# Kernel optimization log

Hardware: AMD Instinct MI355X
Metric: run time of the kernel (lower is better)

## Reference

```python
import jax, jax.numpy as jnp
import numpy as np

N = 100000          # num nodes
E = 1600000         # num edges
IN_F = 256
OUT_F = 256
D_LABEL = 32
ALPHA = 0.2         # LeakyReLU negative slope
EPS = 1e-9


def setup_inputs() -> dict:
    key = jax.random.key(0)
    k1, k2, k3, k4 = jax.random.split(key, 4)
    h = jax.random.normal(k1, (N, IN_F), dtype=jnp.float32)
    label = jax.random.normal(k2, (N, D_LABEL), dtype=jnp.float32)
    # xavier_uniform with gain=1.414 on [IN_F, OUT_F]
    limit = 1.414 * np.sqrt(6.0 / (IN_F + OUT_F))
    W = jax.random.uniform(k3, (IN_F, OUT_F), dtype=jnp.float32,
                           minval=-limit, maxval=limit)
    adj_indices = jax.random.randint(k4, (2, E), 0, N, dtype=jnp.int64)
    return {"h": h, "label": label, "W": W, "adj_indices": adj_indices}


def reference(h, label, W, adj_indices):
    src = adj_indices[0]  # [E]
    dst = adj_indices[1]  # [E]
    Wh = h @ W  # [N, OUT_F]
    # edge attention logits: leakyrelu(<label[src], label[dst]>)
    e = jnp.sum(label[src] * label[dst], axis=1)            # [E]
    e = jnp.where(e >= 0, e, ALPHA * e)                     # LeakyReLU
    # segment softmax over rows (src)
    exp_e = jnp.exp(e)                                      # [E]
    row_sum = jax.ops.segment_sum(exp_e, src, num_segments=N)  # [N]
    row_sum = jnp.maximum(row_sum, EPS)
    att = exp_e / row_sum[src]                              # [E]
    # dropout is identity at inference (training=False)
    # sparse-dense matmul: h_prime[i] = sum_{(i,j) in edges} att * Wh[j]
    msgs = att[:, None] * Wh[dst]                           # [E, OUT_F]
    h_prime = jax.ops.segment_sum(msgs, src, num_segments=N)  # [N, OUT_F]
    return h_prime  # concat=False -> no ELU
```

## Files before the change

kernel.cpp:

```cpp
#include <hip/hip_runtime.h>
#include <hip/hip_bf16.h>

#define NNODES 100000
#define NEDGES 1600000
#define ALPHA  0.2f
#define EPSV   1e-9f

typedef __bf16 bf16x8 __attribute__((ext_vector_type(8)));
typedef float  f32x4  __attribute__((ext_vector_type(4)));
typedef unsigned short u16x8 __attribute__((ext_vector_type(8)));

static __device__ inline unsigned short f2bf(float f) {
    unsigned int u = __float_as_uint(f);
    unsigned int r = u + 0x7fff + ((u >> 16) & 1);
    return (unsigned short)(r >> 16);
}
static __device__ inline float bf2f(unsigned short v) {
    return __uint_as_float((unsigned int)v << 16);
}

__global__ void k_zero(int* __restrict__ p, int n) {
    int i = blockIdx.x * blockDim.x + threadIdx.x;
    if (i < n) p[i] = 0;
}

__global__ void k_prepw(const float* __restrict__ W, unsigned short* __restrict__ Wt) {
    const int i = blockIdx.x * 256 + threadIdx.x;
    const int n = i >> 8, k = i & 255;
    Wt[i] = f2bf(W[k * 256 + n]);
}

#define BM 128
#define BK 32
#define LSTRIDE 40
__global__ __launch_bounds__(256, 2) void k_gemm(const float* __restrict__ h,
                                                 const unsigned short* __restrict__ Wt,
                                                 unsigned short* __restrict__ Wh) {
    __shared__ __align__(16) unsigned short As[BM * LSTRIDE];
    __shared__ __align__(16) unsigned short Bs[256 * LSTRIDE];
    const int tid  = threadIdx.x;
    const int m0   = blockIdx.x * BM;
    const int wave = tid >> 6;
    const int lane = tid & 63;
    const int wm = (wave & 1) * 64;
    const int wn = (wave >> 1) * 128;
    const int fm = lane & 15;
    const int fq = lane >> 4;
    const int fk = fq * 8;

    f32x4 acc[4][8];
    const f32x4 z = {0.f, 0.f, 0.f, 0.f};
#pragma unroll
    for (int i = 0; i < 4; ++i)
#pragma unroll
        for (int j = 0; j < 8; ++j) acc[i][j] = z;

    const int arow = tid >> 1;
    const int acol = (tid & 1) * 16;
    const bool arow_ok = (m0 + arow) < NNODES;
    const float* hrow = h + (size_t)(m0 + arow) * 256 + acol;

    for (int kc = 0; kc < 256; kc += BK) {
        float4 a0, a1, a2, a3;
        if (arow_ok) {
            a0 = *(const float4*)(hrow + kc + 0);
            a1 = *(const float4*)(hrow + kc + 4);
            a2 = *(const float4*)(hrow + kc + 8);
            a3 = *(const float4*)(hrow + kc + 12);
        } else {
            a0 = a1 = a2 = a3 = make_float4(0.f, 0.f, 0.f, 0.f);
        }
        u16x8 bv[4];
#pragma unroll
        for (int q = 0; q < 4; ++q) {
            const int c = tid + 256 * q;
            const int n = c >> 2, koff = (c & 3) * 8;
            bv[q] = *(const u16x8*)(Wt + n * 256 + kc + koff);
        }
        __syncthreads();
        u16x8 p0, p1;
        p0[0]=f2bf(a0.x); p0[1]=f2bf(a0.y); p0[2]=f2bf(a0.z); p0[3]=f2bf(a0.w);
        p0[4]=f2bf(a1.x); p0[5]=f2bf(a1.y); p0[6]=f2bf(a1.z); p0[7]=f2bf(a1.w);
        p1[0]=f2bf(a2.x); p1[1]=f2bf(a2.y); p1[2]=f2bf(a2.z); p1[3]=f2bf(a2.w);
        p1[4]=f2bf(a3.x); p1[5]=f2bf(a3.y); p1[6]=f2bf(a3.z); p1[7]=f2bf(a3.w);
        *(u16x8*)&As[arow * LSTRIDE + acol]     = p0;
        *(u16x8*)&As[arow * LSTRIDE + acol + 8] = p1;
#pragma unroll
        for (int q = 0; q < 4; ++q) {
            const int c = tid + 256 * q;
            const int n = c >> 2, koff = (c & 3) * 8;
            *(u16x8*)&Bs[n * LSTRIDE + koff] = bv[q];
        }
        __syncthreads();
        bf16x8 af[4], bfr[8];
#pragma unroll
        for (int i = 0; i < 4; ++i)
            af[i] = __builtin_bit_cast(bf16x8,
                *(const u16x8*)&As[(wm + 16 * i + fm) * LSTRIDE + fk]);
#pragma unroll
        for (int j = 0; j < 8; ++j)
            bfr[j] = __builtin_bit_cast(bf16x8,
                *(const u16x8*)&Bs[(wn + 16 * j + fm) * LSTRIDE + fk]);
#pragma unroll
        for (int i = 0; i < 4; ++i)
#pragma unroll
            for (int j = 0; j < 8; ++j)
                acc[i][j] = __builtin_amdgcn_mfma_f32_16x16x32_bf16(af[i], bfr[j], acc[i][j], 0, 0, 0);
    }
#pragma unroll
    for (int i = 0; i < 4; ++i) {
#pragma unroll
        for (int r = 0; r < 4; ++r) {
            const int grow = m0 + wm + 16 * i + fq * 4 + r;
            if (grow < NNODES) {
                unsigned short* orow = Wh + (size_t)grow * 256 + wn + fm;
#pragma unroll
                for (int j = 0; j < 8; ++j)
                    orow[16 * j] = f2bf(acc[i][j][r]);
            }
        }
    }
}

__global__ void k_attn(const float* __restrict__ label,
                       const int* __restrict__ src,
                       const int* __restrict__ dst,
                       float* __restrict__ exp_e,
                       int* __restrict__ pos_in_row,
                       int* __restrict__ counts) {
    const int e = blockIdx.x * blockDim.x + threadIdx.x;
    if (e >= NEDGES) return;
    const int s = src[e], d = dst[e];
    const float4* ls = (const float4*)&label[s * 32];
    const float4* ld = (const float4*)&label[d * 32];
    float dot = 0.f;
#pragma unroll
    for (int i = 0; i < 8; ++i) {
        const float4 a = ls[i], b = ld[i];
        dot += a.x * b.x + a.y * b.y + a.z * b.z + a.w * b.w;
    }
    const float lr = dot >= 0.f ? dot : ALPHA * dot;
    exp_e[e] = expf(lr);
    pos_in_row[e] = atomicAdd(&counts[s], 1);
}

__global__ __launch_bounds__(256) void k_scan1(const int* __restrict__ counts,
                                               int* __restrict__ row_start,
                                               int* __restrict__ blockSums) {
    __shared__ int ssum[256];
    const int tid = threadIdx.x;
    const int base = blockIdx.x * 1024 + tid * 4;
    int v[4];
#pragma unroll
    for (int c = 0; c < 4; ++c) v[c] = (base + c < NNODES) ? counts[base + c] : 0;
    const int s = v[0] + v[1] + v[2] + v[3];
    ssum[tid] = s;
    __syncthreads();
    for (int off = 1; off < 256; off <<= 1) {
        const int t = (tid >= off) ? ssum[tid - off] : 0;
        __syncthreads();
        ssum[tid] += t;
        __syncthreads();
    }
    if (tid == 255) blockSums[blockIdx.x] = ssum[255];
    int p = ssum[tid] - s;
#pragma unroll
    for (int c = 0; c < 4; ++c) {
        if (base + c < NNODES) row_start[base + c] = p;
        p += v[c];
    }
}

__global__ __launch_bounds__(256) void k_scan2(int* __restrict__ blockSums, int nb) {
    __shared__ int ssum[256];
    const int tid = threadIdx.x;
    const int s = (tid < nb) ? blockSums[tid] : 0;
    ssum[tid] = s;
    __syncthreads();
    for (int off = 1; off < 256; off <<= 1) {
        const int t = (tid >= off) ? ssum[tid - off] : 0;
        __syncthreads();
        ssum[tid] += t;
        __syncthreads();
    }
    if (tid < nb) blockSums[tid] = ssum[tid] - s;
}

__global__ void k_scan3(int* __restrict__ row_start, const int* __restrict__ blockSums) {
    const int i = blockIdx.x * blockDim.x + threadIdx.x;
    if (i < NNODES) row_start[i] += blockSums[i >> 10];
}

__global__ void k_scatter(const int* __restrict__ src,
                          const int* __restrict__ dst,
                          const float* __restrict__ exp_e,
                          const int* __restrict__ pos_in_row,
                          const int* __restrict__ row_start,
                          int* __restrict__ sorted_dst,
                          float* __restrict__ sorted_w) {
    const int e = blockIdx.x * blockDim.x + threadIdx.x;
    if (e >= NEDGES) return;
    const int pos = row_start[src[e]] + pos_in_row[e];
    sorted_dst[pos] = dst[e];
    sorted_w[pos] = exp_e[e];
}

__global__ __launch_bounds__(256) void k_aggregate(const unsigned short* __restrict__ Wh,
                                                   const int* __restrict__ row_start,
                                                   const int* __restrict__ sorted_dst,
                                                   const float* __restrict__ sorted_w,
                                                   float* __restrict__ out) {
    const int node = blockIdx.x * 4 + (threadIdx.x >> 6);
    if (node >= NNODES) return;
    const int lane = threadIdx.x & 63;
    const int rs = row_start[node];
    const int re = (node == NNODES - 1) ? NEDGES : row_start[node + 1];
    float4 acc = make_float4(0.f, 0.f, 0.f, 0.f);
    float wsum = 0.f;
    for (int i = rs; i < re; ++i) {
        const int d = sorted_dst[i];
        const float w = sorted_w[i];
        wsum += w;
        const ushort4 v = *(const ushort4*)&Wh[(size_t)d * 256 + lane * 4];
        acc.x = fmaf(w, bf2f(v.x), acc.x);
        acc.y = fmaf(w, bf2f(v.y), acc.y);
        acc.z = fmaf(w, bf2f(v.z), acc.z);
        acc.w = fmaf(w, bf2f(v.w), acc.w);
    }
    const float inv = 1.f / fmaxf(wsum, EPSV);
    acc.x *= inv; acc.y *= inv; acc.z *= inv; acc.w *= inv;
    *(float4*)&out[(size_t)node * 256 + lane * 4] = acc;
}

extern "C" void kernel_launch(void* const* d_in, const int* in_sizes, int n_in,
                              void* d_out, int out_size, void* d_ws, size_t ws_size,
                              hipStream_t stream) {
    const float* h     = (const float*)d_in[0];
    const float* label = (const float*)d_in[1];
    const float* W     = (const float*)d_in[2];
    const int*   adj   = (const int*)d_in[3];
    const int* src = adj;
    const int* dst = adj + NEDGES;
    float* out = (float*)d_out;

    char* ws = (char*)d_ws;
    unsigned short* Wh  = (unsigned short*)(ws + 0);
    unsigned short* Wt  = (unsigned short*)(ws + 51200000);
    float* exp_e        = (float*)(ws + 51400000);
    int*   pos_in_row   = (int*)  (ws + 57800000);
    float* sorted_w     = (float*)(ws + 64200000);
    int*   sorted_dst   = (int*)  (ws + 70600000);
    int*   counts       = (int*)  (ws + 77000000);
    int*   row_start    = (int*)  (ws + 77400000);
    int*   blockSums    = (int*)  (ws + 77800000);

    k_zero<<<(NNODES + 255) / 256, 256, 0, stream>>>(counts, NNODES);
    k_prepw<<<256, 256, 0, stream>>>(W, Wt);
    k_gemm<<<(NNODES + BM - 1) / BM, 256, 0, stream>>>(h, Wt, Wh);
    k_attn<<<(NEDGES + 255) / 256, 256, 0, stream>>>(label, src, dst, exp_e, pos_in_row, counts);

    const int nb = (NNODES + 1023) / 1024;
    k_scan1<<<nb, 256, 0, stream>>>(counts, row_start, blockSums);
    k_scan2<<<1, 256, 0, stream>>>(blockSums, nb);
    k_scan3<<<(NNODES + 255) / 256, 256, 0, stream>>>(row_start, blockSums);

    k_scatter<<<(NEDGES + 255) / 256, 256, 0, stream>>>(src, dst, exp_e, pos_in_row,
                                                        row_start, sorted_dst, sorted_w);
    k_aggregate<<<(NNODES + 3) / 4, 256, 0, stream>>>(Wh, row_start, sorted_dst, sorted_w, out);
}
```

Before: 517.1 us.

## Split attention dot across lanes, pack sorted edges, widen aggregate loads

The attention kernel now uses four lanes per edge, each reading 8 label floats, and combines the partial dot products with shuffles so each lane issues fewer, better-coalesced loads. The sorted destination index and weight are packed into a single uint2 array, so each edge needs one 8-byte load. The aggregation kernel maps 32 lanes per node with 16-byte bf16 loads and unrolls the edge loop by 4 to keep more gathers in flight. The trade-off is four times as many threads in the attention launch and higher register use in aggregation.

```diff
diff --git a/kernel.cpp b/kernel.cpp
--- a/kernel.cpp
+++ b/kernel.cpp
@@ -122,26 +122,30 @@
     }
 }
 
-__global__ void k_attn(const float* __restrict__ label,
+__global__ __launch_bounds__(256) void k_attn(const float* __restrict__ label,
                        const int* __restrict__ src,
                        const int* __restrict__ dst,
                        float* __restrict__ exp_e,
                        int* __restrict__ pos_in_row,
                        int* __restrict__ counts) {
-    const int e = blockIdx.x * blockDim.x + threadIdx.x;
+    const int t = blockIdx.x * 256 + threadIdx.x;
+    const int e = t >> 2;
+    const int l4 = t & 3;
     if (e >= NEDGES) return;
     const int s = src[e], d = dst[e];
-    const float4* ls = (const float4*)&label[s * 32];
-    const float4* ld = (const float4*)&label[d * 32];
-    float dot = 0.f;
-#pragma unroll
-    for (int i = 0; i < 8; ++i) {
-        const float4 a = ls[i], b = ld[i];
-        dot += a.x * b.x + a.y * b.y + a.z * b.z + a.w * b.w;
-    }
-    const float lr = dot >= 0.f ? dot : ALPHA * dot;
-    exp_e[e] = expf(lr);
-    pos_in_row[e] = atomicAdd(&counts[s], 1);
+    const float4* ls = (const float4*)&label[s * 32 + l4 * 8];
+    const float4* ld = (const float4*)&label[d * 32 + l4 * 8];
+    const float4 a0 = ls[0], a1 = ls[1];
+    const float4 b0 = ld[0], b1 = ld[1];
+    float dot = a0.x * b0.x + a0.y * b0.y + a0.z * b0.z + a0.w * b0.w
+              + a1.x * b1.x + a1.y * b1.y + a1.z * b1.z + a1.w * b1.w;
+    dot += __shfl_xor(dot, 1);
+    dot += __shfl_xor(dot, 2);
+    if (l4 == 0) {
+        const float lr = dot >= 0.f ? dot : ALPHA * dot;
+        exp_e[e] = expf(lr);
+        pos_in_row[e] = atomicAdd(&counts[s], 1);
+    }
 }
 
 __global__ __launch_bounds__(256) void k_scan1(const int* __restrict__ counts,
@@ -196,40 +200,60 @@
                           const float* __restrict__ exp_e,
                           const int* __restrict__ pos_in_row,
                           const int* __restrict__ row_start,
-                          int* __restrict__ sorted_dst,
-                          float* __restrict__ sorted_w) {
+                          uint2* __restrict__ sorted_pack) {
     const int e = blockIdx.x * blockDim.x + threadIdx.x;
     if (e >= NEDGES) return;
     const int pos = row_start[src[e]] + pos_in_row[e];
-    sorted_dst[pos] = dst[e];
-    sorted_w[pos] = exp_e[e];
+    sorted_pack[pos] = make_uint2((unsigned)dst[e], __float_as_uint(exp_e[e]));
 }
 
 __global__ __launch_bounds__(256) void k_aggregate(const unsigned short* __restrict__ Wh,
                                                    const int* __restrict__ row_start,
-                                                   const int* __restrict__ sorted_dst,
-                                                   const float* __restrict__ sorted_w,
+                                                   const uint2* __restrict__ sorted_pack,
                                                    float* __restrict__ out) {
-    const int node = blockIdx.x * 4 + (threadIdx.x >> 6);
+    const int node = blockIdx.x * 8 + (threadIdx.x >> 5);
     if (node >= NNODES) return;
-    const int lane = threadIdx.x & 63;
+    const int sub = threadIdx.x & 31;
     const int rs = row_start[node];
     const int re = (node == NNODES - 1) ? NEDGES : row_start[node + 1];
-    float4 acc = make_float4(0.f, 0.f, 0.f, 0.f);
+    const unsigned short* __restrict__ Whc = Wh + sub * 8;
+    float acc[8] = {0.f, 0.f, 0.f, 0.f, 0.f, 0.f, 0.f, 0.f};
     float wsum = 0.f;
-    for (int i = rs; i < re; ++i) {
-        const int d = sorted_dst[i];
-        const float w = sorted_w[i];
+    int i = rs;
+    for (; i + 4 <= re; i += 4) {
+        const uint2 p0 = sorted_pack[i + 0];
+        const uint2 p1 = sorted_pack[i + 1];
+        const uint2 p2 = sorted_pack[i + 2];
+        const uint2 p3 = sorted_pack[i + 3];
+        const u16x8 v0 = *(const u16x8*)&Whc[(size_t)p0.x * 256];
+        const u16x8 v1 = *(const u16x8*)&Whc[(size_t)p1.x * 256];
+        const u16x8 v2 = *(const u16x8*)&Whc[(size_t)p2.x * 256];
+        const u16x8 v3 = *(const u16x8*)&Whc[(size_t)p3.x * 256];
+        const float w0 = __uint_as_float(p0.y), w1 = __uint_as_float(p1.y);
+        const float w2 = __uint_as_float(p2.y), w3 = __uint_as_float(p3.y);
+        wsum += (w0 + w1) + (w2 + w3);
+#pragma unroll
+        for (int c = 0; c < 8; ++c) {
+            acc[c] = fmaf(w0, bf2f(v0[c]), acc[c]);
+            acc[c] = fmaf(w1, bf2f(v1[c]), acc[c]);
+            acc[c] = fmaf(w2, bf2f(v2[c]), acc[c]);
+            acc[c] = fmaf(w3, bf2f(v3[c]), acc[c]);
+        }
+    }
+    for (; i < re; ++i) {
+        const uint2 p = sorted_pack[i];
+        const u16x8 v = *(const u16x8*)&Whc[(size_t)p.x * 256];
+        const float w = __uint_as_float(p.y);
         wsum += w;
-        const ushort4 v = *(const ushort4*)&Wh[(size_t)d * 256 + lane * 4];
-        acc.x = fmaf(w, bf2f(v.x), acc.x);
-        acc.y = fmaf(w, bf2f(v.y), acc.y);
-        acc.z = fmaf(w, bf2f(v.z), acc.z);
-        acc.w = fmaf(w, bf2f(v.w), acc.w);
+#pragma unroll
+        for (int c = 0; c < 8; ++c) acc[c] = fmaf(w, bf2f(v[c]), acc[c]);
     }
     const float inv = 1.f / fmaxf(wsum, EPSV);
-    acc.x *= inv; acc.y *= inv; acc.z *= inv; acc.w *= inv;
-    *(float4*)&out[(size_t)node * 256 + lane * 4] = acc;
+    float4 o0 = make_float4(acc[0] * inv, acc[1] * inv, acc[2] * inv, acc[3] * inv);
+    float4 o1 = make_float4(acc[4] * inv, acc[5] * inv, acc[6] * inv, acc[7] * inv);
+    float* orow = out + (size_t)node * 256 + sub * 8;
+    *(float4*)(orow + 0) = o0;
+    *(float4*)(orow + 4) = o1;
 }
 
 extern "C" void kernel_launch(void* const* d_in, const int* in_sizes, int n_in,
@@ -248,8 +272,7 @@
     unsigned short* Wt  = (unsigned short*)(ws + 51200000);
     float* exp_e        = (float*)(ws + 51400000);
     int*   pos_in_row   = (int*)  (ws + 57800000);
-    float* sorted_w     = (float*)(ws + 64200000);
-    int*   sorted_dst   = (int*)  (ws + 70600000);
+    uint2* sorted_pack  = (uint2*)(ws + 64200000);
     int*   counts       = (int*)  (ws + 77000000);
     int*   row_start    = (int*)  (ws + 77400000);
     int*   blockSums    = (int*)  (ws + 77800000);
@@ -257,7 +280,7 @@
     k_zero<<<(NNODES + 255) / 256, 256, 0, stream>>>(counts, NNODES);
     k_prepw<<<256, 256, 0, stream>>>(W, Wt);
     k_gemm<<<(NNODES + BM - 1) / BM, 256, 0, stream>>>(h, Wt, Wh);
-    k_attn<<<(NEDGES + 255) / 256, 256, 0, stream>>>(label, src, dst, exp_e, pos_in_row, counts);
+    k_attn<<<(4 * NEDGES + 255) / 256, 256, 0, stream>>>(label, src, dst, exp_e, pos_in_row, counts);
 
     const int nb = (NNODES + 1023) / 1024;
     k_scan1<<<nb, 256, 0, stream>>>(counts, row_start, blockSums);
@@ -265,6 +288,6 @@
     k_scan3<<<(NNODES + 255) / 256, 256, 0, stream>>>(row_start, blockSums);
 
     k_scatter<<<(NEDGES + 255) / 256, 256, 0, stream>>>(src, dst, exp_e, pos_in_row,
-                                                        row_start, sorted_dst, sorted_w);
-    k_aggregate<<<(NNODES + 3) / 4, 256, 0, stream>>>(Wh, row_start, sorted_dst, sorted_w, out);
-}
+                                                        row_start, sorted_pack);
+    k_aggregate<<<(NNODES + 7) / 8, 256, 0, stream>>>(Wh, row_start, sorted_pack, out);
+}
```

New measurement: 428.9 us. -17.1%, faster.
